# Optimization experiments

Hardware: AMD Instinct MI355X
Metric: run time of the kernel (lower is better)

## Reference

```python
import jax, jax.numpy as jnp
import numpy as np

B, IN, OUT, COND, N, H = 512, 256, 256, 128, 8, 64
DP = max(1, int(OUT * 0.25))          # 64 periodic units (cos+sin -> 2*DP outputs)
DN = OUT - 2 * DP                     # 128 non-periodic units
TPE = IN * DP + IN * DN + DN          # params per expert
TOTAL = N * TPE


def setup_inputs() -> dict:
    key = jax.random.key(0)
    ks = jax.random.split(key, 16)
    s_in = np.sqrt(2.0 / IN).astype(np.float32)
    inp = {
        "x": jax.random.normal(ks[0], (B, IN), jnp.float32),
        "cond": jax.random.normal(ks[1], (B, COND), jnp.float32),
        # expert base weights (torch: randn * sqrt(2/in))
        "base_wp": jax.random.normal(ks[2], (N, IN, DP), jnp.float32) * s_in,
        "base_wn": jax.random.normal(ks[3], (N, IN, DN), jnp.float32) * s_in,
        "base_bn": jnp.zeros((N, DN), jnp.float32),
        # hypernet: Linear(cond,H) -> ReLU -> Linear(H, TOTAL)
        "hW1": jax.random.normal(ks[4], (COND, H), jnp.float32) / np.sqrt(COND),
        "hb1": jnp.zeros((H,), jnp.float32),
        "hW2": jax.random.normal(ks[5], (H, TOTAL), jnp.float32) / np.sqrt(H),
        "hb2": jnp.zeros((TOTAL,), jnp.float32),
        # gating: Linear(cond,3N) -> ReLU -> Linear(3N, N)
        "gW1": jax.random.normal(ks[6], (COND, 3 * N), jnp.float32) / np.sqrt(COND),
        "gb1": jnp.zeros((3 * N,), jnp.float32),
        "gW2": jax.random.normal(ks[7], (3 * N, N), jnp.float32) / np.sqrt(3 * N),
        "gb2": jnp.zeros((N,), jnp.float32),
    }
    return inp


def reference(x, cond, base_wp, base_wn, base_bn,
              hW1, hb1, hW2, hb2, gW1, gb1, gW2, gb2):
    bsz = x.shape[0]
    # hypernet -> per-sample dynamic deltas
    h = jax.nn.relu(cond @ hW1 + hb1)
    delta = (h @ hW2 + hb2).reshape(bsz, N, TPE)
    d_wp = delta[:, :, : IN * DP].reshape(bsz, N, IN, DP)
    d_wn = delta[:, :, IN * DP: IN * DP + IN * DN].reshape(bsz, N, IN, DN)
    d_bn = delta[:, :, IN * DP + IN * DN:]                  # (B, N, DN)

    # periodic branch: per-sample, per-expert mat-vec then cos/sin
    wp = base_wp[None] + d_wp                                # (B,N,IN,DP)
    per = jnp.einsum('bi,bnip->bnp', x, wp)                  # (B,N,DP)
    per_cos, per_sin = jnp.cos(per), jnp.sin(per)

    # non-periodic branch
    wn = base_wn[None] + d_wn                                # (B,N,IN,DN)
    non = jnp.einsum('bi,bnip->bnp', x, wn) + base_bn[None] + d_bn
    non = jax.nn.relu(non)                                   # (B,N,DN)

    # gating over experts
    logits = jax.nn.relu(cond @ gW1 + gb1) @ gW2 + gb2       # (B,N)
    gw = jax.nn.softmax(logits, axis=1)[:, :, None]          # (B,N,1)

    cos_c = jnp.sum(per_cos * gw, axis=1)
    sin_c = jnp.sum(per_sin * gw, axis=1)
    non_c = jnp.sum(non * gw, axis=1)
    return jnp.concatenate([cos_c, sin_c, non_c], axis=-1)   # (B, 2*DP+DN)
```

## Files before the change

kernel.cpp:

```cpp
#include <hip/hip_runtime.h>
#include <math.h>

#define BB     512
#define INF    256
#define CONDF  128
#define NEXP   8
#define HDIM   64
#define TPE    49280
#define TOTC   394240
#define NSPLIT 16
#define CW     1536
#define KB     261

#define AZ_OFF 0u
#define BT_OFF 17104896u
#define P_OFF  68419584u
#define GW_OFF 93585408u
#define CB_OFF 93601792u

typedef __bf16          bf16x8 __attribute__((ext_vector_type(8)));
typedef unsigned short  us8    __attribute__((ext_vector_type(8)));
typedef float           f32x4  __attribute__((ext_vector_type(4)));

__device__ __forceinline__ unsigned short f2bf(float f) {
  unsigned u = __builtin_bit_cast(unsigned, f);
  u += 0x7fffu + ((u >> 16) & 1u);
  return (unsigned short)(u >> 16);
}
__device__ __forceinline__ float bf2f(unsigned short u) {
  return __builtin_bit_cast(float, ((unsigned)u) << 16);
}

__device__ __forceinline__ void gld16(const void* g, const void* l) {
  __builtin_amdgcn_global_load_lds(
      (const __attribute__((address_space(1))) unsigned int*)g,
      (__attribute__((address_space(3))) unsigned int*)l, 16, 0, 0);
}

__global__ __launch_bounds__(256, 4)
void k_bt(const float* __restrict__ hW2, unsigned short* __restrict__ Bt,
          const float* __restrict__ bwp, const float* __restrict__ bwn,
          const float* __restrict__ bbn, const float* __restrict__ hb2,
          float* __restrict__ colbias,
          const float* __restrict__ x, const float* __restrict__ cond,
          const float* __restrict__ hW1, const float* __restrict__ hb1,
          const float* __restrict__ gW1, const float* __restrict__ gb1,
          const float* __restrict__ gW2, const float* __restrict__ gb2,
          unsigned short* __restrict__ Az, float* __restrict__ gw) {
  const int bx = blockIdx.x;
  const int tid = threadIdx.x;
  __shared__ __align__(16) unsigned short Ls[64 * 256];

  if (bx >= 2072) {
    const int ne = bx - 2072;
    unsigned short* L2 = Ls;
#pragma unroll
    for (int it = 0; it < 8; ++it) {
      const int f = it * 256 + tid;
      const int t = f >> 5, c4 = (f & 31) * 4;
      f32x4 v = *(const f32x4*)(hW2 + (size_t)t * TOTC + (size_t)ne * TPE + 49152 + c4);
#pragma unroll
      for (int j = 0; j < 4; ++j) L2[t * 129 + c4 + j] = f2bf(v[j]);
    }
    if (tid < 192)
      colbias[ne * 192 + tid] = (tid < 64) ? 0.f
        : bbn[ne * 128 + (tid - 64)] + hb2[(size_t)ne * TPE + 49152 + (tid - 64)];
    __syncthreads();
    if (tid < 128) {
      const int c = tid;
#pragma unroll
      for (int t8 = 0; t8 < 8; ++t8) {
        us8 o;
#pragma unroll
        for (int j = 0; j < 8; ++j) o[j] = L2[(t8 * 8 + j) * 129 + c];
        *(us8*)(Bt + ((size_t)260 * CW + ne * 192 + 64 + c) * 64 + t8 * 8) = o;
      }
    } else {
      const int cz = (tid - 128) >> 1, hf = (tid - 128) & 1;
      us8 z = (us8){0, 0, 0, 0, 0, 0, 0, 0};
#pragma unroll
      for (int t8 = 0; t8 < 4; ++t8)
        *(us8*)(Bt + ((size_t)260 * CW + ne * 192 + cz) * 64 + (hf * 4 + t8) * 8) = z;
    }
    return;
  }

  if (bx >= 1536 && bx < 2048) {
    const int b = bx - 1536;
    float* xs  = (float*)Ls;
    float* cs  = xs + INF;
    float* hs  = cs + CONDF;
    float* g1  = hs + HDIM;
    float* lsb = g1 + 24;
    float* es  = lsb + 8;
    xs[tid] = x[b * INF + tid];
    if (tid < CONDF) cs[tid] = cond[b * CONDF + tid];
    __syncthreads();
    if (tid < HDIM) {
      float acc = hb1[tid];
      for (int q = 0; q < CONDF; ++q) acc = fmaf(cs[q], hW1[q * HDIM + tid], acc);
      hs[tid] = fmaxf(acc, 0.f);
    }
    if (tid >= 64 && tid < 88) {
      const int r = tid - 64;
      float acc = gb1[r];
      for (int q = 0; q < CONDF; ++q) acc = fmaf(cs[q], gW1[q * 24 + r], acc);
      g1[r] = fmaxf(acc, 0.f);
    }
    __syncthreads();
    if (tid < NEXP) {
      float acc = gb2[tid];
      for (int j = 0; j < 24; ++j) acc = fmaf(g1[j], gW2[j * NEXP + tid], acc);
      lsb[tid] = acc;
    }
    __syncthreads();
    if (tid < NEXP) {
      float m = lsb[0];
      for (int j = 1; j < NEXP; ++j) m = fmaxf(m, lsb[j]);
      es[tid] = expf(lsb[tid] - m);
    }
    __syncthreads();
    if (tid < NEXP) {
      float s = 0.f;
      for (int j = 0; j < NEXP; ++j) s += es[j];
      gw[b * NEXP + tid] = es[tid] / s;
    }
    const int t0 = tid >> 5, ig = tid & 31;
#pragma unroll
    for (int tt = 0; tt < 8; ++tt) {
      const int t = tt * 8 + t0;
      const float hv = hs[t];
      us8 o;
#pragma unroll
      for (int j = 0; j < 8; ++j) o[j] = f2bf(hv * xs[ig * 8 + j]);
      *(us8*)(Az + ((size_t)(t * 4 + (ig >> 3)) * BB + b) * 64 + (ig & 7) * 8) = o;
    }
    Az[((size_t)(256 + (tid >> 6)) * BB + b) * 64 + (tid & 63)] = f2bf(xs[tid]);
    if (tid < HDIM) Az[((size_t)260 * BB + b) * 64 + tid] = f2bf(hs[tid]);
    return;
  }

  const int pq = tid & 15, rg = tid >> 4, p4 = pq * 4;
  int kbBase, cbase;

  if (bx < 1536) {
    const int t = bx / 24, rem = bx % 24, ne = rem / 3, sec = rem % 3;
    const int dst  = sec ? 128 : 64;
    const int poff = (sec == 2) ? 64 : 0;
    kbBase = t * 4;
    cbase  = ne * 192 + sec * 64;
    const float* src = hW2 + (size_t)t * TOTC + (size_t)ne * TPE
                       + (sec ? 16384 : 0) + poff + p4;
    f32x4 va[8], vb[8];
#pragma unroll
    for (int it = 0; it < 8; ++it) {
      const int i0 = rg * 2 + it * 32;
      va[it] = *(const f32x4*)(src + (size_t)i0 * dst);
      vb[it] = *(const f32x4*)(src + (size_t)(i0 + 1) * dst);
    }
#pragma unroll
    for (int it = 0; it < 8; ++it) {
      const int i0 = rg * 2 + it * 32;
      const int e = i0 >> 3, q0 = i0 & 7;
#pragma unroll
      for (int j = 0; j < 4; ++j) {
        const int p = p4 + j;
        const unsigned lo = f2bf(va[it][j]), hi = f2bf(vb[it][j]);
        *(unsigned*)(&Ls[(p << 8) + (((e ^ (p >> 2)) << 3) | q0)]) = lo | (hi << 16);
      }
    }
  } else {
    const int u = bx - 2048, ne = u / 3, sec = u % 3;
    const int dst  = sec ? 128 : 64;
    const int poff = (sec == 2) ? 64 : 0;
    kbBase = 256;
    cbase  = ne * 192 + sec * 64;
    const float* s1 = sec ? (bwn + (size_t)ne * INF * 128 + poff)
                          : (bwp + (size_t)ne * INF * 64);
    const float* s2 = hb2 + (size_t)ne * TPE + (sec ? 16384 : 0) + poff;
#pragma unroll
    for (int it = 0; it < 8; ++it) {
      const int i0 = rg * 2 + it * 32;
      f32x4 a1 = *(const f32x4*)(s1 + (size_t)i0 * dst + p4);
      f32x4 a2 = *(const f32x4*)(s2 + (size_t)i0 * dst + p4);
      f32x4 b1 = *(const f32x4*)(s1 + (size_t)(i0 + 1) * dst + p4);
      f32x4 b2 = *(const f32x4*)(s2 + (size_t)(i0 + 1) * dst + p4);
      const int e = i0 >> 3, q0 = i0 & 7;
#pragma unroll
      for (int j = 0; j < 4; ++j) {
        const int p = p4 + j;
        const unsigned lo = f2bf(a1[j] + a2[j]);
        const unsigned hi = f2bf(b1[j] + b2[j]);
        *(unsigned*)(&Ls[(p << 8) + (((e ^ (p >> 2)) << 3) | q0)]) = lo | (hi << 16);
      }
    }
  }
  __syncthreads();
  us8 o[8];
#pragma unroll
  for (int it2 = 0; it2 < 8; ++it2) {
    const int of = it2 * 256 + tid;
    const int p = of >> 5, seg = of & 31;
    o[it2] = *(const us8*)(&Ls[(p << 8) + ((seg ^ (p >> 2)) << 3)]);
  }
#pragma unroll
  for (int it2 = 0; it2 < 8; ++it2) {
    const int of = it2 * 256 + tid;
    const int p = of >> 5, seg = of & 31, ib = seg >> 3, k8 = seg & 7;
    *(us8*)(Bt + ((size_t)(kbBase + ib) * CW + cbase + p) * 64 + k8 * 8) = o[it2];
  }
}

__launch_bounds__(256, 3)
__global__ void k_gemm(const unsigned short* __restrict__ Az,
                       const unsigned short* __restrict__ Bt,
                       unsigned short* __restrict__ P) {
  const int bid = blockIdx.x;
  const int g  = (bid >> 5) * 8 + (bid & 7);
  const int mt = (bid >> 3) & 3;
  const int nt = g >> 4;
  const int s  = g & 15;
  const int m0 = mt * 128, n0 = nt * 128;
  const int kb0 = s * 16 + (s < 5 ? s : 5);
  const int kb1 = kb0 + 16 + (s < 5 ? 1 : 0);
  const int tid = threadIdx.x;
  __shared__ __align__(16) unsigned short As[128 * 64];
  __shared__ __align__(16) unsigned short Bs[128 * 64];

  f32x4 acc[4][4];
#pragma unroll
  for (int mi = 0; mi < 4; ++mi)
#pragma unroll
    for (int ni = 0; ni < 4; ++ni) acc[mi][ni] = (f32x4){0.f, 0.f, 0.f, 0.f};

  const int wv = tid >> 6, lane = tid & 63;
  const int wm = wv >> 1, wn = wv & 1;
  const int lrow = lane & 15, quad = lane >> 4;
  const int srow = tid >> 3;
  const int sg0  = tid & 7;

  const unsigned short* ab = Az + ((size_t)kb0 * BB + m0) * 64;
  const unsigned short* bb = Bt + ((size_t)kb0 * CW + n0) * 64;

  for (int kb = kb0; kb < kb1; ++kb) {
#pragma unroll
    for (int it = 0; it < 4; ++it) {
      const int r = it * 32 + srow;
      const int ga = sg0 ^ (r & 7);
      const int ldsoff = __builtin_amdgcn_readfirstlane(it * 4096 + wv * 1024);
      gld16(ab + (size_t)r * 64 + ga * 8, (const char*)As + ldsoff);
      gld16(bb + (size_t)r * 64 + ga * 8, (const char*)Bs + ldsoff);
    }
    __syncthreads();
#pragma unroll
    for (int kh = 0; kh < 2; ++kh) {
      bf16x8 af[4], bfr[4];
#pragma unroll
      for (int mi = 0; mi < 4; ++mi) {
        const int r = wm * 64 + mi * 16 + lrow;
        const int ga = (kh * 4 + quad) ^ (r & 7);
        af[mi] = *(const bf16x8*)(As + r * 64 + ga * 8);
      }
#pragma unroll
      for (int ni = 0; ni < 4; ++ni) {
        const int r = wn * 64 + ni * 16 + lrow;
        const int ga = (kh * 4 + quad) ^ (r & 7);
        bfr[ni] = *(const bf16x8*)(Bs + r * 64 + ga * 8);
      }
#pragma unroll
      for (int mi = 0; mi < 4; ++mi)
#pragma unroll
        for (int ni = 0; ni < 4; ++ni)
          acc[mi][ni] = __builtin_amdgcn_mfma_f32_16x16x32_bf16(af[mi], bfr[ni], acc[mi][ni], 0, 0, 0);
    }
    __syncthreads();
    ab += (size_t)BB * 64;
    bb += (size_t)CW * 64;
  }

#pragma unroll
  for (int mi = 0; mi < 4; ++mi) {
    const int row0 = m0 + wm * 64 + mi * 16 + quad * 4;
#pragma unroll
    for (int ni = 0; ni < 4; ++ni) {
      const int col = n0 + wn * 64 + ni * 16 + lrow;
      unsigned short* pp = P + ((size_t)s * BB + row0) * CW + col;
#pragma unroll
      for (int r = 0; r < 4; ++r) pp[(size_t)r * CW] = f2bf(acc[mi][ni][r]);
    }
  }
}

__global__ __launch_bounds__(256, 8)
void k_epi(const unsigned short* __restrict__ P, const float* __restrict__ gw,
           const float* __restrict__ colbias, float* __restrict__ out) {
  const int b = blockIdx.x;
  const int t = threadIdx.x;
  __shared__ float cc[NEXP][64];
  __shared__ float ss[NEXP][64];
  __shared__ float nn[NEXP][128];
  __shared__ float gws[NEXP];
  if (t < NEXP) gws[t] = gw[b * NEXP + t];
  __syncthreads();
  if (t < 192) {
    const int n = t / 24, rr = (t % 24) * 8;
    const int c = n * 192 + rr;
    float acc[8];
#pragma unroll
    for (int j = 0; j < 8; ++j) acc[j] = colbias[c + j];
#pragma unroll
    for (int s2 = 0; s2 < NSPLIT; ++s2) {
      us8 v = *(const us8*)(P + ((size_t)s2 * BB + b) * CW + c);
#pragma unroll
      for (int j = 0; j < 8; ++j) acc[j] += bf2f(v[j]);
    }
    const float gv = gws[n];
    if (rr < 64) {
#pragma unroll
      for (int j = 0; j < 8; ++j) {
        cc[n][rr + j] = gv * cosf(acc[j]);
        ss[n][rr + j] = gv * sinf(acc[j]);
      }
    } else {
#pragma unroll
      for (int j = 0; j < 8; ++j)
        nn[n][rr - 64 + j] = gv * fmaxf(acc[j], 0.f);
    }
  }
  __syncthreads();
  float sum = 0.f;
  if (t < 64) {
#pragma unroll
    for (int n = 0; n < NEXP; ++n) sum += cc[n][t];
  } else if (t < 128) {
#pragma unroll
    for (int n = 0; n < NEXP; ++n) sum += ss[n][t - 64];
  } else {
#pragma unroll
    for (int n = 0; n < NEXP; ++n) sum += nn[n][t - 128];
  }
  out[b * 256 + t] = sum;
}

extern "C" void kernel_launch(void* const* d_in, const int* in_sizes, int n_in,
                              void* d_out, int out_size, void* d_ws, size_t ws_size,
                              hipStream_t stream) {
  const float* x    = (const float*)d_in[0];
  const float* cond = (const float*)d_in[1];
  const float* bwp  = (const float*)d_in[2];
  const float* bwn  = (const float*)d_in[3];
  const float* bbn  = (const float*)d_in[4];
  const float* hW1  = (const float*)d_in[5];
  const float* hb1  = (const float*)d_in[6];
  const float* hW2  = (const float*)d_in[7];
  const float* hb2  = (const float*)d_in[8];
  const float* gW1  = (const float*)d_in[9];
  const float* gb1  = (const float*)d_in[10];
  const float* gW2  = (const float*)d_in[11];
  const float* gb2  = (const float*)d_in[12];
  float* out = (float*)d_out;
  char* ws = (char*)d_ws;

  unsigned short* Az = (unsigned short*)(ws + AZ_OFF);
  unsigned short* Bt = (unsigned short*)(ws + BT_OFF);
  unsigned short* Pp = (unsigned short*)(ws + P_OFF);
  float* gw      = (float*)(ws + GW_OFF);
  float* colbias = (float*)(ws + CB_OFF);

  hipLaunchKernelGGL(k_bt, dim3(2080), dim3(256), 0, stream,
                     hW2, Bt, bwp, bwn, bbn, hb2, colbias,
                     x, cond, hW1, hb1, gW1, gb1, gW2, gb2, Az, gw);
  hipLaunchKernelGGL(k_gemm, dim3(768), dim3(256), 0, stream, Az, Bt, Pp);
  hipLaunchKernelGGL(k_epi, dim3(BB), dim3(256), 0, stream, Pp, gw, colbias, out);
}
```

Before: 213.9 us.

## Stage hW2 tiles via global_load_lds and overlap second half with flush

The hW2-to-bf16 transpose blocks in k_bt now load fp32 rows directly into LDS with global_load_lds, using an XOR-swizzled layout, instead of going through registers. Each block works in two halves of 128 rows, and the load of the second half overlaps the global store of the first. The goal is to cut register pressure and raise memory-level parallelism in this bandwidth-bound prep kernel. In exchange, LDS use grows to 48 KB and the launch-bounds occupancy hint drops from 4 to 3, which may lower achieved occupancy.

```diff
diff --git a/kernel.cpp b/kernel.cpp
--- a/kernel.cpp
+++ b/kernel.cpp
@@ -37,7 +37,7 @@
       (__attribute__((address_space(3))) unsigned int*)l, 16, 0, 0);
 }
 
-__global__ __launch_bounds__(256, 4)
+__global__ __launch_bounds__(256, 3)
 void k_bt(const float* __restrict__ hW2, unsigned short* __restrict__ Bt,
           const float* __restrict__ bwp, const float* __restrict__ bwn,
           const float* __restrict__ bbn, const float* __restrict__ hb2,
@@ -49,11 +49,11 @@
           unsigned short* __restrict__ Az, float* __restrict__ gw) {
   const int bx = blockIdx.x;
   const int tid = threadIdx.x;
-  __shared__ __align__(16) unsigned short Ls[64 * 256];
+  __shared__ __align__(16) char smem[49152];
 
   if (bx >= 2072) {
     const int ne = bx - 2072;
-    unsigned short* L2 = Ls;
+    unsigned short* L2 = (unsigned short*)smem;
 #pragma unroll
     for (int it = 0; it < 8; ++it) {
       const int f = it * 256 + tid;
@@ -87,7 +87,7 @@
 
   if (bx >= 1536 && bx < 2048) {
     const int b = bx - 1536;
-    float* xs  = (float*)Ls;
+    float* xs  = (float*)smem;
     float* cs  = xs + INF;
     float* hs  = cs + CONDF;
     float* g1  = hs + HDIM;
@@ -140,41 +140,13 @@
     return;
   }
 
-  const int pq = tid & 15, rg = tid >> 4, p4 = pq * 4;
-  int kbBase, cbase;
-
-  if (bx < 1536) {
-    const int t = bx / 24, rem = bx % 24, ne = rem / 3, sec = rem % 3;
-    const int dst  = sec ? 128 : 64;
-    const int poff = (sec == 2) ? 64 : 0;
-    kbBase = t * 4;
-    cbase  = ne * 192 + sec * 64;
-    const float* src = hW2 + (size_t)t * TOTC + (size_t)ne * TPE
-                       + (sec ? 16384 : 0) + poff + p4;
-    f32x4 va[8], vb[8];
-#pragma unroll
-    for (int it = 0; it < 8; ++it) {
-      const int i0 = rg * 2 + it * 32;
-      va[it] = *(const f32x4*)(src + (size_t)i0 * dst);
-      vb[it] = *(const f32x4*)(src + (size_t)(i0 + 1) * dst);
-    }
-#pragma unroll
-    for (int it = 0; it < 8; ++it) {
-      const int i0 = rg * 2 + it * 32;
-      const int e = i0 >> 3, q0 = i0 & 7;
-#pragma unroll
-      for (int j = 0; j < 4; ++j) {
-        const int p = p4 + j;
-        const unsigned lo = f2bf(va[it][j]), hi = f2bf(vb[it][j]);
-        *(unsigned*)(&Ls[(p << 8) + (((e ^ (p >> 2)) << 3) | q0)]) = lo | (hi << 16);
-      }
-    }
-  } else {
+  if (bx >= 2048) {
+    unsigned short* Ls = (unsigned short*)smem;
+    const int pq = tid & 15, rg = tid >> 4, p4 = pq * 4;
     const int u = bx - 2048, ne = u / 3, sec = u % 3;
     const int dst  = sec ? 128 : 64;
     const int poff = (sec == 2) ? 64 : 0;
-    kbBase = 256;
-    cbase  = ne * 192 + sec * 64;
+    const int cbase = ne * 192 + sec * 64;
     const float* s1 = sec ? (bwn + (size_t)ne * INF * 128 + poff)
                           : (bwp + (size_t)ne * INF * 64);
     const float* s2 = hb2 + (size_t)ne * TPE + (sec ? 16384 : 0) + poff;
@@ -194,21 +166,97 @@
         *(unsigned*)(&Ls[(p << 8) + (((e ^ (p >> 2)) << 3) | q0)]) = lo | (hi << 16);
       }
     }
-  }
-  __syncthreads();
-  us8 o[8];
-#pragma unroll
-  for (int it2 = 0; it2 < 8; ++it2) {
-    const int of = it2 * 256 + tid;
-    const int p = of >> 5, seg = of & 31;
-    o[it2] = *(const us8*)(&Ls[(p << 8) + ((seg ^ (p >> 2)) << 3)]);
-  }
-#pragma unroll
-  for (int it2 = 0; it2 < 8; ++it2) {
-    const int of = it2 * 256 + tid;
-    const int p = of >> 5, seg = of & 31, ib = seg >> 3, k8 = seg & 7;
-    *(us8*)(Bt + ((size_t)(kbBase + ib) * CW + cbase + p) * 64 + k8 * 8) = o[it2];
-  }
+    __syncthreads();
+    us8 o[8];
+#pragma unroll
+    for (int it2 = 0; it2 < 8; ++it2) {
+      const int of = it2 * 256 + tid;
+      const int p = of >> 5, seg = of & 31;
+      o[it2] = *(const us8*)(&Ls[(p << 8) + ((seg ^ (p >> 2)) << 3)]);
+    }
+#pragma unroll
+    for (int it2 = 0; it2 < 8; ++it2) {
+      const int of = it2 * 256 + tid;
+      const int p = of >> 5, seg = of & 31, ib = seg >> 3, k8 = seg & 7;
+      *(us8*)(Bt + ((size_t)(256 + ib) * CW + cbase + p) * 64 + k8 * 8) = o[it2];
+    }
+    return;
+  }
+
+  const int t = bx / 24, rem = bx % 24, ne = rem / 3, sec = rem % 3;
+  const int dstB = sec ? 512 : 256;
+  const int poff = (sec == 2) ? 64 : 0;
+  const int kbBase = t * 4;
+  const int cbase  = ne * 192 + sec * 64;
+  const char* Sb = (const char*)(hW2 + (size_t)t * TOTC + (size_t)ne * TPE
+                                 + (sec ? 16384 : 0) + poff);
+  float* Lf = (float*)smem;
+  unsigned short* Lo = (unsigned short*)(smem + 32768);
+  const int wv = tid >> 6, lane = tid & 63;
+  const int pq = tid & 15, rg = tid >> 4;
+
+#define STAGE(ih)                                                             \
+  {                                                                           \
+    _Pragma("unroll")                                                         \
+    for (int j = 0; j < 8; ++j) {                                             \
+      const int row = wv * 32 + j * 4 + (lane >> 4);                          \
+      const int scol = (lane & 15) ^ (((row >> 1) & 1) << 3);                 \
+      const int ldsoff = __builtin_amdgcn_readfirstlane(wv * 8192 + j * 1024);\
+      gld16(Sb + (size_t)((ih) * 128 + row) * dstB + scol * 16,               \
+            (const char*)Lf + ldsoff);                                        \
+    }                                                                         \
+  }
+
+#define XPOSE()                                                               \
+  {                                                                           \
+    _Pragma("unroll")                                                         \
+    for (int it2 = 0; it2 < 4; ++it2) {                                       \
+      const int li0 = rg * 2 + it2 * 32;                     \
+      const int cg = pq ^ (((li0 >> 1) & 1) << 3);                            \
+      f32x4 a = *(const f32x4*)((const char*)Lf + li0 * 256 + cg * 16);       \
+      f32x4 b = *(const f32x4*)((const char*)Lf + (li0 + 1) * 256 + cg * 16); \
+      const int e4 = li0 >> 3, q0 = li0 & 7;                                  \
+      _Pragma("unroll")                                                       \
+      for (int j = 0; j < 4; ++j) {                                           \
+        const int p = pq * 4 + j;                                             \
+        const unsigned lo = f2bf(a[j]), hi = f2bf(b[j]);                      \
+        *(unsigned*)((char*)Lo + p * 256 + (((e4 ^ pq) << 4) | (q0 << 1)))    \
+            = lo | (hi << 16);                                                \
+      }                                                                       \
+    }                                                                         \
+  }
+
+#define FLUSH(ih)                                                             \
+  {                                                                           \
+    us8 o[4];                                                                 \
+    _Pragma("unroll")                                                         \
+    for (int it3 = 0; it3 < 4; ++it3) {                                       \
+      const int of = it3 * 256 + tid;                                         \
+      const int p = of >> 4, e4 = of & 15;                                    \
+      o[it3] = *(const us8*)((const char*)Lo + p * 256 + ((e4 ^ (p >> 2)) << 4)); \
+    }                                                                         \
+    _Pragma("unroll")                                                         \
+    for (int it3 = 0; it3 < 4; ++it3) {                                       \
+      const int of = it3 * 256 + tid;                                         \
+      const int p = of >> 4, e4 = of & 15;                                    \
+      *(us8*)(Bt + ((size_t)(kbBase + (ih) * 2 + (e4 >> 3)) * CW + cbase + p) * 64 \
+              + (e4 & 7) * 8) = o[it3];                                       \
+    }                                                                         \
+  }
+
+  STAGE(0);
+  __syncthreads();
+  XPOSE();
+  __syncthreads();
+  STAGE(1);
+  FLUSH(0);
+  __syncthreads();
+  XPOSE();
+  __syncthreads();
+  FLUSH(1);
+#undef STAGE
+#undef XPOSE
+#undef FLUSH
 }
 
 __launch_bounds__(256, 3)
```

New measurement: 216.5 us. Within noise of the previous version (+1.2%).

## Split hW2 transpose into dedicated kernel using direct global-to-LDS loads

Applied to the files above, without the earlier changes.

The main hW2 fp32-to-bf16 transpose blocks are moved out of the combined prep kernel into a separate kernel. It uses global_load_lds to stream fp32 rows straight into a 64KB XOR-swizzled LDS tile, then converts and writes transposed bf16. The remaining small jobs (Az/gating, base weights, bias rows) go into a second prep kernel. The aim is to raise memory throughput on the dominant 100MB hW2 read. The cost is an extra launch and lower occupancy from the larger LDS tile.

```diff
diff --git a/kernel.cpp b/kernel.cpp
--- a/kernel.cpp
+++ b/kernel.cpp
@@ -37,57 +37,65 @@
       (__attribute__((address_space(3))) unsigned int*)l, 16, 0, 0);
 }
 
-__global__ __launch_bounds__(256, 4)
-void k_bt(const float* __restrict__ hW2, unsigned short* __restrict__ Bt,
-          const float* __restrict__ bwp, const float* __restrict__ bwn,
-          const float* __restrict__ bbn, const float* __restrict__ hb2,
-          float* __restrict__ colbias,
-          const float* __restrict__ x, const float* __restrict__ cond,
-          const float* __restrict__ hW1, const float* __restrict__ hb1,
-          const float* __restrict__ gW1, const float* __restrict__ gb1,
-          const float* __restrict__ gW2, const float* __restrict__ gb2,
-          unsigned short* __restrict__ Az, float* __restrict__ gw) {
+__global__ __launch_bounds__(256, 2)
+void k_tr(const float* __restrict__ hW2, unsigned short* __restrict__ Bt) {
   const int bx = blockIdx.x;
   const int tid = threadIdx.x;
-  __shared__ __align__(16) unsigned short Ls[64 * 256];
-
-  if (bx >= 2072) {
-    const int ne = bx - 2072;
-    unsigned short* L2 = Ls;
-#pragma unroll
-    for (int it = 0; it < 8; ++it) {
-      const int f = it * 256 + tid;
-      const int t = f >> 5, c4 = (f & 31) * 4;
-      f32x4 v = *(const f32x4*)(hW2 + (size_t)t * TOTC + (size_t)ne * TPE + 49152 + c4);
-#pragma unroll
-      for (int j = 0; j < 4; ++j) L2[t * 129 + c4 + j] = f2bf(v[j]);
-    }
-    if (tid < 192)
-      colbias[ne * 192 + tid] = (tid < 64) ? 0.f
-        : bbn[ne * 128 + (tid - 64)] + hb2[(size_t)ne * TPE + 49152 + (tid - 64)];
-    __syncthreads();
-    if (tid < 128) {
-      const int c = tid;
-#pragma unroll
-      for (int t8 = 0; t8 < 8; ++t8) {
-        us8 o;
-#pragma unroll
-        for (int j = 0; j < 8; ++j) o[j] = L2[(t8 * 8 + j) * 129 + c];
-        *(us8*)(Bt + ((size_t)260 * CW + ne * 192 + 64 + c) * 64 + t8 * 8) = o;
-      }
-    } else {
-      const int cz = (tid - 128) >> 1, hf = (tid - 128) & 1;
-      us8 z = (us8){0, 0, 0, 0, 0, 0, 0, 0};
-#pragma unroll
-      for (int t8 = 0; t8 < 4; ++t8)
-        *(us8*)(Bt + ((size_t)260 * CW + ne * 192 + cz) * 64 + (hf * 4 + t8) * 8) = z;
-    }
-    return;
-  }
-
-  if (bx >= 1536 && bx < 2048) {
-    const int b = bx - 1536;
-    float* xs  = (float*)Ls;
+  __shared__ __align__(16) char smem[65536];
+  float* Lf = (float*)smem;
+  const int t = bx / 24, rem = bx % 24, ne = rem / 3, sec = rem % 3;
+  const int dstB = sec ? 512 : 256;
+  const int poff = (sec == 2) ? 64 : 0;
+  const int kbBase = t * 4;
+  const int cbase  = ne * 192 + sec * 64;
+  const char* Sb = (const char*)(hW2 + (size_t)t * TOTC + (size_t)ne * TPE
+                                 + (sec ? 16384 : 0) + poff);
+  const int wv = tid >> 6, lane = tid & 63;
+
+#pragma unroll
+  for (int ih = 0; ih < 2; ++ih)
+#pragma unroll
+    for (int j = 0; j < 8; ++j) {
+      const int row = wv * 32 + j * 4 + (lane >> 4);
+      const int scol = (lane & 15) ^ ((row >> 3) & 15);
+      const int ldsoff = __builtin_amdgcn_readfirstlane(
+          ih * 32768 + wv * 8192 + j * 1024);
+      gld16(Sb + (size_t)(ih * 128 + row) * dstB + scol * 16, smem + ldsoff);
+    }
+  __syncthreads();
+
+#pragma unroll
+  for (int it = 0; it < 8; ++it) {
+    const int of = it * 256 + tid;
+    const int k8 = of & 7, p = (of >> 3) & 63, ib = of >> 9;
+    const int s = (ib * 8 + k8) & 15;
+    const int base = (((p >> 2) ^ s) << 4) + (p & 3) * 4;
+    const char* rp = (const char*)Lf + (size_t)(ib * 64 + k8 * 8) * 256 + base;
+    us8 o;
+#pragma unroll
+    for (int jj = 0; jj < 8; ++jj)
+      o[jj] = f2bf(*(const float*)(rp + jj * 256));
+    *(us8*)(Bt + ((size_t)(kbBase + ib) * CW + cbase + p) * 64 + k8 * 8) = o;
+  }
+}
+
+__global__ __launch_bounds__(256, 4)
+void k_prep(const float* __restrict__ hW2, unsigned short* __restrict__ Bt,
+            const float* __restrict__ bwp, const float* __restrict__ bwn,
+            const float* __restrict__ bbn, const float* __restrict__ hb2,
+            float* __restrict__ colbias,
+            const float* __restrict__ x, const float* __restrict__ cond,
+            const float* __restrict__ hW1, const float* __restrict__ hb1,
+            const float* __restrict__ gW1, const float* __restrict__ gb1,
+            const float* __restrict__ gW2, const float* __restrict__ gb2,
+            unsigned short* __restrict__ Az, float* __restrict__ gw) {
+  const int bx = blockIdx.x;
+  const int tid = threadIdx.x;
+  __shared__ __align__(16) char smem[32768];
+
+  if (bx < 512) {
+    const int b = bx;
+    float* xs  = (float*)smem;
     float* cs  = xs + INF;
     float* hs  = cs + CONDF;
     float* g1  = hs + HDIM;
@@ -140,41 +148,47 @@
     return;
   }
 
-  const int pq = tid & 15, rg = tid >> 4, p4 = pq * 4;
-  int kbBase, cbase;
-
-  if (bx < 1536) {
-    const int t = bx / 24, rem = bx % 24, ne = rem / 3, sec = rem % 3;
+  if (bx >= 536) {
+    const int ne = bx - 536;
+    unsigned short* L2 = (unsigned short*)smem;
+#pragma unroll
+    for (int it = 0; it < 8; ++it) {
+      const int f = it * 256 + tid;
+      const int t = f >> 5, c4 = (f & 31) * 4;
+      f32x4 v = *(const f32x4*)(hW2 + (size_t)t * TOTC + (size_t)ne * TPE + 49152 + c4);
+#pragma unroll
+      for (int j = 0; j < 4; ++j) L2[t * 129 + c4 + j] = f2bf(v[j]);
+    }
+    if (tid < 192)
+      colbias[ne * 192 + tid] = (tid < 64) ? 0.f
+        : bbn[ne * 128 + (tid - 64)] + hb2[(size_t)ne * TPE + 49152 + (tid - 64)];
+    __syncthreads();
+    if (tid < 128) {
+      const int c = tid;
+#pragma unroll
+      for (int t8 = 0; t8 < 8; ++t8) {
+        us8 o;
+#pragma unroll
+        for (int j = 0; j < 8; ++j) o[j] = L2[(t8 * 8 + j) * 129 + c];
+        *(us8*)(Bt + ((size_t)260 * CW + ne * 192 + 64 + c) * 64 + t8 * 8) = o;
+      }
+    } else {
+      const int cz = (tid - 128) >> 1, hf = (tid - 128) & 1;
+      us8 z = (us8){0, 0, 0, 0, 0, 0, 0, 0};
+#pragma unroll
+      for (int t8 = 0; t8 < 4; ++t8)
+        *(us8*)(Bt + ((size_t)260 * CW + ne * 192 + cz) * 64 + (hf * 4 + t8) * 8) = z;
+    }
+    return;
+  }
+
+  {
+    unsigned short* Ls = (unsigned short*)smem;
+    const int pq = tid & 15, rg = tid >> 4, p4 = pq * 4;
+    const int u = bx - 512, ne = u / 3, sec = u % 3;
     const int dst  = sec ? 128 : 64;
     const int poff = (sec == 2) ? 64 : 0;
-    kbBase = t * 4;
-    cbase  = ne * 192 + sec * 64;
-    const float* src = hW2 + (size_t)t * TOTC + (size_t)ne * TPE
-                       + (sec ? 16384 : 0) + poff + p4;
-    f32x4 va[8], vb[8];
-#pragma unroll
-    for (int it = 0; it < 8; ++it) {
-      const int i0 = rg * 2 + it * 32;
-      va[it] = *(const f32x4*)(src + (size_t)i0 * dst);
-      vb[it] = *(const f32x4*)(src + (size_t)(i0 + 1) * dst);
-    }
-#pragma unroll
-    for (int it = 0; it < 8; ++it) {
-      const int i0 = rg * 2 + it * 32;
-      const int e = i0 >> 3, q0 = i0 & 7;
-#pragma unroll
-      for (int j = 0; j < 4; ++j) {
-        const int p = p4 + j;
-        const unsigned lo = f2bf(va[it][j]), hi = f2bf(vb[it][j]);
-        *(unsigned*)(&Ls[(p << 8) + (((e ^ (p >> 2)) << 3) | q0)]) = lo | (hi << 16);
-      }
-    }
-  } else {
-    const int u = bx - 2048, ne = u / 3, sec = u % 3;
-    const int dst  = sec ? 128 : 64;
-    const int poff = (sec == 2) ? 64 : 0;
-    kbBase = 256;
-    cbase  = ne * 192 + sec * 64;
+    const int cbase = ne * 192 + sec * 64;
     const float* s1 = sec ? (bwn + (size_t)ne * INF * 128 + poff)
                           : (bwp + (size_t)ne * INF * 64);
     const float* s2 = hb2 + (size_t)ne * TPE + (sec ? 16384 : 0) + poff;
@@ -194,20 +208,20 @@
         *(unsigned*)(&Ls[(p << 8) + (((e ^ (p >> 2)) << 3) | q0)]) = lo | (hi << 16);
       }
     }
-  }
-  __syncthreads();
-  us8 o[8];
-#pragma unroll
-  for (int it2 = 0; it2 < 8; ++it2) {
-    const int of = it2 * 256 + tid;
-    const int p = of >> 5, seg = of & 31;
-    o[it2] = *(const us8*)(&Ls[(p << 8) + ((seg ^ (p >> 2)) << 3)]);
-  }
-#pragma unroll
-  for (int it2 = 0; it2 < 8; ++it2) {
-    const int of = it2 * 256 + tid;
-    const int p = of >> 5, seg = of & 31, ib = seg >> 3, k8 = seg & 7;
-    *(us8*)(Bt + ((size_t)(kbBase + ib) * CW + cbase + p) * 64 + k8 * 8) = o[it2];
+    __syncthreads();
+    us8 o[8];
+#pragma unroll
+    for (int it2 = 0; it2 < 8; ++it2) {
+      const int of = it2 * 256 + tid;
+      const int p = of >> 5, seg = of & 31;
+      o[it2] = *(const us8*)(&Ls[(p << 8) + ((seg ^ (p >> 2)) << 3)]);
+    }
+#pragma unroll
+    for (int it2 = 0; it2 < 8; ++it2) {
+      const int of = it2 * 256 + tid;
+      const int p = of >> 5, seg = of & 31, ib = seg >> 3, k8 = seg & 7;
+      *(us8*)(Bt + ((size_t)(256 + ib) * CW + cbase + p) * 64 + k8 * 8) = o[it2];
+    }
   }
 }
 
@@ -367,7 +381,8 @@
   float* gw      = (float*)(ws + GW_OFF);
   float* colbias = (float*)(ws + CB_OFF);
 
-  hipLaunchKernelGGL(k_bt, dim3(2080), dim3(256), 0, stream,
+  hipLaunchKernelGGL(k_tr,   dim3(1536), dim3(256), 0, stream, hW2, Bt);
+  hipLaunchKernelGGL(k_prep, dim3(544),  dim3(256), 0, stream,
                      hW2, Bt, bwp, bwn, bbn, hb2, colbias,
                      x, cond, hW1, hb1, gW1, gb1, gW2, gb2, Az, gw);
   hipLaunchKernelGGL(k_gemm, dim3(768), dim3(256), 0, stream, Az, Bt, Pp);
```

Result: slower. 220.4 us (+3.0%).
